# Kernel optimization log

Hardware: AMD Instinct MI355X
Metric: run time of the kernel (lower is better)

The kernel has to match this reference:

```python
import jax, jax.numpy as jnp
import numpy as np

B, L, D = 2, 1536, 1024
H, P = 16, 1024
HD = P // H  # 64
K_SIZE = 5
DIFF_STEPS = 3
ALPHA = 0.02
NEG = -1e9
EPS = 1e-9


def setup_inputs() -> dict:
    key = jax.random.key(0)
    ks = jax.random.split(key, 12)
    s = 0.02
    hidden_states = jax.random.normal(ks[0], (B, L, D), dtype=jnp.float32)
    attention_mask = jax.random.randint(ks[1], (B, L), 0, 2, dtype=jnp.int32)
    Wq = jax.random.normal(ks[2], (D, P), dtype=jnp.float32) * s
    bq = jax.random.normal(ks[3], (P,), dtype=jnp.float32) * s
    Wk = jax.random.normal(ks[4], (D, P), dtype=jnp.float32) * s
    bk = jax.random.normal(ks[5], (P,), dtype=jnp.float32) * s
    Wv = jax.random.normal(ks[6], (D, P), dtype=jnp.float32) * s
    bv = jax.random.normal(ks[7], (P,), dtype=jnp.float32) * s
    Wo = jax.random.normal(ks[8], (P, D), dtype=jnp.float32) * s
    bo = jax.random.normal(ks[9], (D,), dtype=jnp.float32) * s
    kernel_w = jax.random.normal(ks[10], (K_SIZE,), dtype=jnp.float32)
    return {"hidden_states": hidden_states, "attention_mask": attention_mask,
            "Wq": Wq, "bq": bq, "Wk": Wk, "bk": bk, "Wv": Wv, "bv": bv,
            "Wo": Wo, "bo": bo, "kernel_w": kernel_w}


def _causal_smooth(p, w):
    # p: (B,H,Lq,Lk); causal cross-correlation matching F.conv1d(pad=k-1)[:Lk]
    k = w.shape[0]
    Lk = p.shape[-1]
    pp = jnp.pad(p, ((0, 0), (0, 0), (0, 0), (k - 1, 0)))
    out = w[0] * pp[..., 0:Lk]
    for j in range(1, k):
        out = out + w[j] * pp[..., j:j + Lk]
    return out


def reference(hidden_states, attention_mask, Wq, bq, Wk, bk, Wv, bv, Wo, bo, kernel_w):
    mask_f = attention_mask.astype(hidden_states.dtype)  # (B,Lk), 1=keep
    additive = (1.0 - mask_f) * NEG                       # (B,Lk)
    key_valid = (attention_mask > 0).astype(hidden_states.dtype)

    Q = (hidden_states @ Wq + bq).reshape(B, L, H, HD)
    Kt = (hidden_states @ Wk + bk).reshape(B, L, H, HD)
    V = (hidden_states @ Wv + bv).reshape(B, L, H, HD)

    scores = jnp.einsum('bqhd,bkhd->bhqk', Q, Kt) / np.sqrt(HD).astype(np.float32)
    scores = scores + additive[:, None, None, :]
    p = jax.nn.softmax(scores, axis=-1)  # (B,H,Lq,Lk)

    w = jax.nn.softmax(kernel_w)  # (k,)
    kv4 = key_valid[:, None, None, :]
    for _ in range(DIFF_STEPS):
        ps = _causal_smooth(p, w)
        ps = ps * kv4
        ps = ps / (jnp.sum(ps, axis=-1, keepdims=True) + EPS)
        p = (1.0 - ALPHA) * p + ALPHA * ps

    attn = jnp.einsum('bhqk,bkhd->bqhd', p, V).reshape(B, L, P)
    return attn @ Wo + bo
```

## Files before the change

kernel.cpp:

```cpp
#include <hip/hip_runtime.h>

#define BB 2
#define LL 1536
#define DD 1024
#define HH 16
#define HDD 64
#define PP 1024

typedef __attribute__((ext_vector_type(8))) __bf16 bf16x8;
typedef __attribute__((ext_vector_type(4))) float f32x4;
typedef __attribute__((ext_vector_type(2))) float f32x2;
typedef _Float16 f16x2 __attribute__((ext_vector_type(2)));

__device__ __forceinline__ unsigned short f2b(float f) {
  unsigned int x = __builtin_bit_cast(unsigned int, f);
  unsigned int r = (x + 0x7FFFu + ((x >> 16) & 1u)) >> 16;
  return (unsigned short)r;
}
__device__ __forceinline__ bf16x8 ldb8(const unsigned short* p) {
  return __builtin_bit_cast(bf16x8, *(const uint4*)p);
}
__device__ __forceinline__ f32x2 mk2(float a, float b) {
  f32x2 r;
  r.x = a;
  r.y = b;
  return r;
}
__device__ __forceinline__ unsigned int cvtpk_bf16(float lo, float hi) {
  unsigned int r;
  asm("v_cvt_pk_bf16_f32 %0, %1, %2" : "=v"(r) : "v"(lo), "v"(hi));
  return r;
}
__device__ __forceinline__ float fdot2u(unsigned int a, unsigned int ones,
                                        float c) {
#if __has_builtin(__builtin_amdgcn_fdot2)
  return __builtin_amdgcn_fdot2(__builtin_bit_cast(f16x2, a),
                                __builtin_bit_cast(f16x2, ones), c, false);
#else
  f16x2 x = __builtin_bit_cast(f16x2, a);
  return c + (float)x.x + (float)x.y;
#endif
}
__device__ __forceinline__ void gl_lds16(const unsigned short* g,
                                         unsigned short* l) {
  __builtin_amdgcn_global_load_lds(
      (const __attribute__((address_space(1))) void*)g,
      (__attribute__((address_space(3))) void*)l, 16, 0, 0);
}

__global__ __launch_bounds__(256) void prep(
    const float* __restrict__ hs, unsigned short* __restrict__ hsb,
    const float* __restrict__ Wq, const float* __restrict__ Wk,
    const float* __restrict__ Wv, const float* __restrict__ Wo,
    unsigned short* __restrict__ WT) {
  const int bid = blockIdx.x;
  const int t = threadIdx.x;
  if (bid < 1536) {
    const int idx = bid * 2048 + t * 8;
    float4 a = *(const float4*)(hs + idx);
    float4 b = *(const float4*)(hs + idx + 4);
    uint4 u;
    u.x = (unsigned int)f2b(a.x) | ((unsigned int)f2b(a.y) << 16);
    u.y = (unsigned int)f2b(a.z) | ((unsigned int)f2b(a.w) << 16);
    u.z = (unsigned int)f2b(b.x) | ((unsigned int)f2b(b.y) << 16);
    u.w = (unsigned int)f2b(b.z) | ((unsigned int)f2b(b.w) << 16);
    *(uint4*)(hsb + idx) = u;
  } else {
    __shared__ float tile[64][68];
    const int t2 = bid - 1536;
    const int z = t2 >> 8;
    const int bx = t2 & 15, by = (t2 >> 4) & 15;
    const float* W = (z == 0) ? Wq : (z == 1) ? Wk : (z == 2) ? Wv : Wo;
    unsigned short* O = WT + (size_t)z * 1024 * 1024;
    const int r0 = by * 64;
    const int c0 = bx * 64;
#pragma unroll
    for (int i = 0; i < 4; ++i) {
      const int row = (t >> 4) + i * 16;
      const int col = (t & 15) * 4;
      *(float4*)&tile[row][col] =
          *(const float4*)&W[(size_t)(r0 + row) * 1024 + c0 + col];
    }
    __syncthreads();
#pragma unroll
    for (int i = 0; i < 4; ++i) {
      const int n = (t >> 4) + i * 16;
      const int k4 = (t & 15) * 4;
      uint2 u;
      u.x = (unsigned int)f2b(tile[k4 + 0][n]) |
            ((unsigned int)f2b(tile[k4 + 1][n]) << 16);
      u.y = (unsigned int)f2b(tile[k4 + 2][n]) |
            ((unsigned int)f2b(tile[k4 + 3][n]) << 16);
      *(uint2*)&O[(size_t)(c0 + n) * 1024 + r0 + k4] = u;
    }
  }
}

template <int MODE>
__device__ __forceinline__ void gemm_mfma_body(
    const unsigned short* __restrict__ A, const unsigned short* __restrict__ Bt,
    const float* __restrict__ bias, void* __restrict__ Cout) {
  __shared__ unsigned short As[128 * 32];
  __shared__ unsigned short Bs[128 * 32];
  const int t = threadIdx.x;
  const int lane = t & 63;
  const int w = t >> 6;
  const int quad = lane >> 4;
  const int lc = lane & 15;
  const int m0 = blockIdx.y * 128, n0 = blockIdx.x * 128;

  const int sr = lane >> 2;
  const int sk = (lane & 3) * 8;
  const unsigned short* ga0 = A + (size_t)(m0 + w * 32 + sr) * 1024 + sk;
  const unsigned short* ga1 = ga0 + 16 * 1024;
  const unsigned short* gb0 = Bt + (size_t)(n0 + w * 32 + sr) * 1024 + sk;
  const unsigned short* gb1 = gb0 + 16 * 1024;
  unsigned short* la0 = As + w * 1024;
  unsigned short* la1 = As + w * 1024 + 512;
  unsigned short* lb0 = Bs + w * 1024;
  unsigned short* lb1 = Bs + w * 1024 + 512;

  const int mrow0 = (w >> 1) * 64, ncol0 = (w & 1) * 64;

  f32x4 acc[4][4];
#pragma unroll
  for (int i = 0; i < 4; ++i)
#pragma unroll
    for (int j = 0; j < 4; ++j) acc[i][j] = (f32x4){0.f, 0.f, 0.f, 0.f};

  for (int k0 = 0; k0 < 1024; k0 += 32) {
    __syncthreads();
    gl_lds16(ga0 + k0, la0);
    gl_lds16(ga1 + k0, la1);
    gl_lds16(gb0 + k0, lb0);
    gl_lds16(gb1 + k0, lb1);
    __syncthreads();
    bf16x8 af[4], bfr[4];
#pragma unroll
    for (int i = 0; i < 4; ++i)
      af[i] = ldb8(&As[(mrow0 + i * 16 + lc) * 32 + quad * 8]);
#pragma unroll
    for (int j = 0; j < 4; ++j)
      bfr[j] = ldb8(&Bs[(ncol0 + j * 16 + lc) * 32 + quad * 8]);
#pragma unroll
    for (int i = 0; i < 4; ++i)
#pragma unroll
      for (int j = 0; j < 4; ++j)
        acc[i][j] = __builtin_amdgcn_mfma_f32_16x16x32_bf16(af[i], bfr[j],
                                                            acc[i][j], 0, 0, 0);
  }

#pragma unroll
  for (int i = 0; i < 4; ++i) {
    const int row0 = m0 + mrow0 + i * 16 + quad * 4;
#pragma unroll
    for (int jj = 0; jj < 4; ++jj) {
      const int col = n0 + ncol0 + jj * 16 + lc;
      const float bz = bias[col];
      float o[4];
#pragma unroll
      for (int r = 0; r < 4; ++r) o[r] = acc[i][jj][r] + bz;
      if constexpr (MODE == 0) {
        const int bb = row0 / LL;
        const int ql = row0 - bb * LL;
        const int qt = ql >> 4;
        const int m = ql & 15;
        const int hh = col >> 6;
        const int hd = col & 63;
        const int f = hd >> 5;
        const int qk = (hd >> 3) & 3;
        const int j = hd & 7;
        unsigned short* QF = (unsigned short*)Cout;
        const size_t base = (((size_t)(bb * HH + hh) * 96 + qt) * 2 + f) * 512 +
                            (qk * 16 + m) * 8 + j;
#pragma unroll
        for (int r = 0; r < 4; ++r) QF[base + r * 8] = f2b(o[r] * 0.125f);
      } else if constexpr (MODE == 1) {
        const int bb = row0 / LL;
        const int kl = row0 - bb * LL;
        const int ktl = kl >> 4;
        const int m = kl & 15;
        const int hh = col >> 6;
        const int hd = col & 63;
        const int f = hd >> 5;
        const int qk = (hd >> 3) & 3;
        const int j = hd & 7;
        unsigned short* KF = (unsigned short*)Cout;
        const size_t base =
            (((size_t)(bb * HH + hh) * 96 + ktl) * 2 + f) * 512 +
            (qk * 16 + m) * 8 + j;
#pragma unroll
        for (int r = 0; r < 4; ++r) KF[base + r * 8] = f2b(o[r]);
      } else if constexpr (MODE == 2) {
        const int bb = row0 / LL;
        const int kl = row0 - bb * LL;
        const int hh = col >> 6;
        const int hd = col & 63;
        const int hg = hd >> 4;
        const int lcv = hd & 15;
        const int tile = (kl >> 5);
        const int qv = (kl >> 3) & 3;
        const int j0 = kl & 7;
        unsigned short* VF = (unsigned short*)Cout;
        const size_t base = (((size_t)(bb * HH + hh) * 4 + hg) * 48 + tile) * 512 +
                            (qv * 16 + lcv) * 8 + j0;
        uint2 u;
        u.x = (unsigned int)f2b(o[0]) | ((unsigned int)f2b(o[1]) << 16);
        u.y = (unsigned int)f2b(o[2]) | ((unsigned int)f2b(o[3]) << 16);
        *(uint2*)&VF[base] = u;
      } else {
#pragma unroll
        for (int r = 0; r < 4; ++r)
          ((float*)Cout)[(size_t)(row0 + r) * 1024 + col] = o[r];
      }
    }
  }
}

__global__ __launch_bounds__(256) void qkv_gemm(
    const unsigned short* __restrict__ hsb,
    const unsigned short* __restrict__ WT, const float* __restrict__ bq,
    const float* __restrict__ bk, const float* __restrict__ bv,
    unsigned short* __restrict__ QF, unsigned short* __restrict__ KF,
    unsigned short* __restrict__ VF) {
  if (blockIdx.z == 0) {
    gemm_mfma_body<0>(hsb, WT, bq, QF);
  } else if (blockIdx.z == 1) {
    gemm_mfma_body<1>(hsb, WT + 1024 * 1024, bk, KF);
  } else {
    gemm_mfma_body<2>(hsb, WT + 2 * 1024 * 1024, bv, VF);
  }
}

__global__ __launch_bounds__(256) void out_gemm(
    const unsigned short* __restrict__ ctxb,
    const unsigned short* __restrict__ WoT, const float* __restrict__ bo,
    float* __restrict__ out) {
  gemm_mfma_body<3>(ctxb, WoT, bo, out);
}

__global__ __launch_bounds__(1024, 2) void attn_kernel(
    const unsigned short* __restrict__ QF,
    const unsigned short* __restrict__ KF,
    const unsigned short* __restrict__ VF, const int* __restrict__ mask,
    const float* __restrict__ kernel_w, unsigned short* __restrict__ ctxb) {
  __shared__ __align__(16) unsigned int P2u[97 * 128];
  __shared__ unsigned int kvb[48];
  __shared__ float red_s[16][16];
  __shared__ float wext[48];

  const int t = threadIdx.x;
  const int lane = t & 63;
  const int w = t >> 6;
  const int quad = lane >> 4;
  const int lc = lane & 15;
  const int b = blockIdx.z, h = blockIdx.y;
  const int q0 = blockIdx.x * 16;

  {
    unsigned long long bal = __ballot(mask[b * LL + t] > 0);
    if (lane == 0) {
      kvb[2 * w] = (unsigned int)bal;
      kvb[2 * w + 1] = (unsigned int)(bal >> 32);
    }
  }
  if (w < 8) {
    unsigned long long bal = __ballot(mask[b * LL + 1024 + t] > 0);
    if (lane == 0) {
      kvb[32 + 2 * w] = (unsigned int)bal;
      kvb[33 + 2 * w] = (unsigned int)(bal >> 32);
    }
  }
  if (t < 128) P2u[t] = 0;
  {
    float k0 = kernel_w[0], k1 = kernel_w[1], k2 = kernel_w[2],
          k3 = kernel_w[3], k4 = kernel_w[4];
    float km = fmaxf(fmaxf(fmaxf(k0, k1), fmaxf(k2, k3)), k4);
    float e0 = __expf(k0 - km), e1 = __expf(k1 - km), e2 = __expf(k2 - km),
          e3 = __expf(k3 - km), e4 = __expf(k4 - km);
    float es = e0 + e1 + e2 + e3 + e4;
    if (t < 48) {
      float v = 0.f;
      if (t == 16) v = e4 / es;
      if (t == 17) v = e3 / es;
      if (t == 18) v = e2 / es;
      if (t == 19) v = e1 / es;
      if (t == 20) v = e0 / es;
      wext[t] = v;
    }
  }
  __syncthreads();

  bf16x8 afb;
  {
    const int kb = lc + 32 - quad * 8;
    float bv[8];
#pragma unroll
    for (int jj = 0; jj < 8; ++jj) bv[jj] = wext[kb - jj];
    uint4 uu;
    uu.x = cvtpk_bf16(bv[0], bv[1]);
    uu.y = cvtpk_bf16(bv[2], bv[3]);
    uu.z = cvtpk_bf16(bv[4], bv[5]);
    uu.w = cvtpk_bf16(bv[6], bv[7]);
    afb = __builtin_bit_cast(bf16x8, uu);
  }

  const unsigned short* qfb =
      QF + (((size_t)(b * HH + h) * 96 + (q0 >> 4)) * 2) * 512 + lane * 8;
  const bf16x8 qb0 = ldb8(qfb);
  const bf16x8 qb1 = ldb8(qfb + 512);
  const unsigned short* kfb =
      KF + (((size_t)(b * HH + h) * 96 + 6 * w) * 2) * 512 + lane * 8;
  f32x2 pr[12];
#pragma unroll
  for (int j = 0; j < 6; ++j) {
    bf16x8 ka0 = ldb8(kfb + j * 1024);
    bf16x8 ka1 = ldb8(kfb + j * 1024 + 512);
    f32x4 acc = {0.f, 0.f, 0.f, 0.f};
    acc = __builtin_amdgcn_mfma_f32_16x16x32_bf16(ka0, qb0, acc, 0, 0, 0);
    acc = __builtin_amdgcn_mfma_f32_16x16x32_bf16(ka1, qb1, acc, 0, 0, 0);
    pr[2 * j] = mk2(acc[0], acc[1]);
    pr[2 * j + 1] = mk2(acc[2], acc[3]);
  }

  unsigned int mA = 0u;
  float s = 0.f;
#pragma unroll
  for (int j = 0; j < 6; ++j) {
    const int kb16 = 16 * j + 4 * quad;
    const unsigned int w4 = (kvb[3 * w + (kb16 >> 5)] >> (kb16 & 31)) & 0xFu;
    mA |= w4 << (4 * j);
    float e0 = (w4 & 1u) ? __expf(pr[2 * j].x) : 0.f;
    float e1 = (w4 & 2u) ? __expf(pr[2 * j].y) : 0.f;
    float e2 = (w4 & 4u) ? __expf(pr[2 * j + 1].x) : 0.f;
    float e3 = (w4 & 8u) ? __expf(pr[2 * j + 1].y) : 0.f;
    pr[2 * j] = mk2(e0, e1);
    pr[2 * j + 1] = mk2(e2, e3);
    s += (e0 + e1) + (e2 + e3);
  }
  s += __shfl_xor(s, 16, 64);
  s += __shfl_xor(s, 32, 64);
  if (lane < 16) red_s[w][lane] = s;
  __syncthreads();
  float tot0 = 0.f;
#pragma unroll
  for (int ww = 0; ww < 16; ++ww) tot0 += red_s[ww][lc];
  const float inv = 1.f / tot0;
#pragma unroll
  for (int i = 0; i < 12; ++i) pr[i] = pr[i] * inv;

  unsigned int* const pwb = &P2u[((6 * w + 1) * 16 + lc) * 8 + 2 * quad];
#pragma unroll
  for (int j = 0; j < 6; ++j) {
    uint2 u;
    u.x = cvtpk_bf16(pr[2 * j].x, pr[2 * j].y);
    u.y = cvtpk_bf16(pr[2 * j + 1].x, pr[2 * j + 1].y);
    *(uint2*)(pwb + j * 128) = u;
  }
  __syncthreads();

  const unsigned int ones2 = 0x3C003C00u;
  const unsigned int* const prb =
      &P2u[((6 * w + (quad >> 1)) * 16 + lc) * 8 + (quad & 1) * 4];
#pragma unroll
  for (int step = 0; step < 3; ++step) {
    unsigned int s_pk[12];
    float sum = 0.f;
#pragma unroll
    for (int j = 0; j < 6; ++j) {
      bf16x8 bfr = ldb8((const unsigned short*)(prb + j * 128));
      f32x4 z = {0.f, 0.f, 0.f, 0.f};
      f32x4 ps = __builtin_amdgcn_mfma_f32_16x16x32_bf16(afb, bfr, z, 0, 0, 0);
      const unsigned int w4 = (mA >> (4 * j)) & 0xFu;
      float p0 = (w4 & 1u) ? ps[0] : 0.f;
      float p1 = (w4 & 2u) ? ps[1] : 0.f;
      float p2 = (w4 & 4u) ? ps[2] : 0.f;
      float p3 = (w4 & 8u) ? ps[3] : 0.f;
      s_pk[2 * j] =
          __builtin_bit_cast(unsigned int, __builtin_amdgcn_cvt_pkrtz(p0, p1));
      s_pk[2 * j + 1] =
          __builtin_bit_cast(unsigned int, __builtin_amdgcn_cvt_pkrtz(p2, p3));
      sum = fdot2u(s_pk[2 * j], ones2, sum);
      sum = fdot2u(s_pk[2 * j + 1], ones2, sum);
    }
    sum += __shfl_xor(sum, 16, 64);
    sum += __shfl_xor(sum, 32, 64);
    if (lane < 16) red_s[w][lane] = sum;
    __syncthreads();
    float tot = 0.f;
#pragma unroll
    for (int ww = 0; ww < 16; ++ww) tot += red_s[ww][lc];
    const float pinv = 0.02f / (tot + 1e-9f);
#pragma unroll
    for (int i = 0; i < 12; ++i) {
      f16x2 hp = __builtin_bit_cast(f16x2, s_pk[i]);
      pr[i] = pr[i] * 0.98f + mk2((float)hp.x, (float)hp.y) * pinv;
    }
#pragma unroll
    for (int j = 0; j < 6; ++j) {
      uint2 u;
      u.x = cvtpk_bf16(pr[2 * j].x, pr[2 * j].y);
      u.y = cvtpk_bf16(pr[2 * j + 1].x, pr[2 * j + 1].y);
      *(uint2*)(pwb + j * 128) = u;
    }
    __syncthreads();
  }

  const int cg = w & 3;
  const int kt = w >> 2;
  const int cidx = cg * 16 + lc;
  const unsigned short* vfb =
      VF + ((((size_t)(b * HH + h) * 4 + cg) * 48 + 12 * kt) * 512) + lane * 8;
  const unsigned int* const pvb =
      &P2u[((24 * kt + 1 + (quad >> 1)) * 16 + lc) * 8 + (quad & 1) * 4];
  f32x4 oacc = {0.f, 0.f, 0.f, 0.f};
#pragma unroll
  for (int g = 0; g < 6; ++g) {
#pragma unroll
    for (int c = 0; c < 2; ++c) {
      bf16x8 pa = ldb8((const unsigned short*)(pvb + (4 * g + 2 * c) * 128));
      bf16x8 vf = ldb8(vfb + (2 * g + c) * 512);
      oacc = __builtin_amdgcn_mfma_f32_16x16x32_bf16(pa, vf, oacc, 0, 0, 0);
    }
  }
  __syncthreads();
  float* pscr = (float*)&P2u[0];
  if (kt > 0) {
    const int idx = (kt - 1) * 4096 + ((cg * 4 + quad) * 16 + lc) * 4;
    *(float4*)(pscr + idx) = make_float4(oacc[0], oacc[1], oacc[2], oacc[3]);
  }
  __syncthreads();
  if (kt == 0) {
    float o[4] = {oacc[0], oacc[1], oacc[2], oacc[3]};
#pragma unroll
    for (int p = 0; p < 3; ++p) {
      const int idx = p * 4096 + ((cg * 4 + quad) * 16 + lc) * 4;
      float4 prr = *(const float4*)(pscr + idx);
      o[0] += prr.x;
      o[1] += prr.y;
      o[2] += prr.z;
      o[3] += prr.w;
    }
#pragma unroll
    for (int r = 0; r < 4; ++r)
      ctxb[((size_t)(b * LL + q0 + quad * 4 + r)) * PP + h * HDD + cidx] =
          f2b(o[r]);
  }
}

extern "C" void kernel_launch(void* const* d_in, const int* in_sizes, int n_in,
                              void* d_out, int out_size, void* d_ws,
                              size_t ws_size, hipStream_t stream) {
  const float* hs = (const float*)d_in[0];
  const int* mask = (const int*)d_in[1];
  const float* Wq = (const float*)d_in[2];
  const float* bq = (const float*)d_in[3];
  const float* Wk = (const float*)d_in[4];
  const float* bk = (const float*)d_in[5];
  const float* Wv = (const float*)d_in[6];
  const float* bv = (const float*)d_in[7];
  const float* Wo = (const float*)d_in[8];
  const float* bo = (const float*)d_in[9];
  const float* kw = (const float*)d_in[10];

  const size_t NBLP = (size_t)BB * LL * PP;
  unsigned short* QF = (unsigned short*)d_ws;
  unsigned short* KF = QF + NBLP;
  unsigned short* VF = KF + NBLP;
  unsigned short* ctxb = VF + NBLP;
  unsigned short* hsb = ctxb + NBLP;
  unsigned short* WT = hsb + NBLP;

  dim3 blk(256);
  prep<<<dim3(2560), blk, 0, stream>>>(hs, hsb, Wq, Wk, Wv, Wo, WT);
  qkv_gemm<<<dim3(8, 24, 3), blk, 0, stream>>>(hsb, WT, bq, bk, bv, QF, KF, VF);
  attn_kernel<<<dim3(96, 16, 2), dim3(1024), 0, stream>>>(QF, KF, VF, mask, kw,
                                                          ctxb);
  out_gemm<<<dim3(8, 24, 1), blk, 0, stream>>>(ctxb, WT + 3 * 1024 * 1024, bo,
                                               (float*)d_out);
}
```

Before: 280.2 us.

## Switch attention diffusion to fp16 packed math and defer softmax normalization

Attention probabilities are now kept as packed fp16 in registers, and the diffusion update uses packed f16x2 arithmetic instead of fp32 with bf16 repacking. The smoothing and PV matmuls move from bf16 MFMA to f16 MFMA, and V is stored as fp16. The softmax normalization no longer has its own barrier: the unnormalized exponentials are written first and scaled inside the first diffusion step, using double-buffered reduction arrays. This removes one barrier and many conversion instructions, at the cost of fp16 range and precision risks, since unnormalized exps can overflow fp16.

After: 276.3 us. No clear change (-1.4%).

```diff
diff --git a/kernel.cpp b/kernel.cpp
--- a/kernel.cpp
+++ b/kernel.cpp
@@ -11,6 +11,7 @@
 typedef __attribute__((ext_vector_type(4))) float f32x4;
 typedef __attribute__((ext_vector_type(2))) float f32x2;
 typedef _Float16 f16x2 __attribute__((ext_vector_type(2)));
+typedef _Float16 f16x8 __attribute__((ext_vector_type(8)));
 
 __device__ __forceinline__ unsigned short f2b(float f) {
   unsigned int x = __builtin_bit_cast(unsigned int, f);
@@ -19,6 +20,9 @@
 }
 __device__ __forceinline__ bf16x8 ldb8(const unsigned short* p) {
   return __builtin_bit_cast(bf16x8, *(const uint4*)p);
+}
+__device__ __forceinline__ f16x8 ldh8u(const unsigned int* p) {
+  return __builtin_bit_cast(f16x8, *(const uint4*)p);
 }
 __device__ __forceinline__ f32x2 mk2(float a, float b) {
   f32x2 r;
@@ -26,10 +30,8 @@
   r.y = b;
   return r;
 }
-__device__ __forceinline__ unsigned int cvtpk_bf16(float lo, float hi) {
-  unsigned int r;
-  asm("v_cvt_pk_bf16_f32 %0, %1, %2" : "=v"(r) : "v"(lo), "v"(hi));
-  return r;
+__device__ __forceinline__ unsigned int pkrtz(float lo, float hi) {
+  return __builtin_bit_cast(unsigned int, __builtin_amdgcn_cvt_pkrtz(lo, hi));
 }
 __device__ __forceinline__ float fdot2u(unsigned int a, unsigned int ones,
                                         float c) {
@@ -205,8 +207,8 @@
         const size_t base = (((size_t)(bb * HH + hh) * 4 + hg) * 48 + tile) * 512 +
                             (qv * 16 + lcv) * 8 + j0;
         uint2 u;
-        u.x = (unsigned int)f2b(o[0]) | ((unsigned int)f2b(o[1]) << 16);
-        u.y = (unsigned int)f2b(o[2]) | ((unsigned int)f2b(o[3]) << 16);
+        u.x = pkrtz(o[0], o[1]);
+        u.y = pkrtz(o[2], o[3]);
         *(uint2*)&VF[base] = u;
       } else {
 #pragma unroll
@@ -246,7 +248,8 @@
     const float* __restrict__ kernel_w, unsigned short* __restrict__ ctxb) {
   __shared__ __align__(16) unsigned int P2u[97 * 128];
   __shared__ unsigned int kvb[48];
-  __shared__ float red_s[16][16];
+  __shared__ float red_a[16][16];
+  __shared__ float red_b[16][16];
   __shared__ float wext[48];
 
   const int t = threadIdx.x;
@@ -291,18 +294,15 @@
   }
   __syncthreads();
 
-  bf16x8 afb;
+  f16x8 afb;
   {
     const int kb = lc + 32 - quad * 8;
-    float bv[8];
-#pragma unroll
-    for (int jj = 0; jj < 8; ++jj) bv[jj] = wext[kb - jj];
     uint4 uu;
-    uu.x = cvtpk_bf16(bv[0], bv[1]);
-    uu.y = cvtpk_bf16(bv[2], bv[3]);
-    uu.z = cvtpk_bf16(bv[4], bv[5]);
-    uu.w = cvtpk_bf16(bv[6], bv[7]);
-    afb = __builtin_bit_cast(bf16x8, uu);
+    uu.x = pkrtz(wext[kb], wext[kb - 1]);
+    uu.y = pkrtz(wext[kb - 2], wext[kb - 3]);
+    uu.z = pkrtz(wext[kb - 4], wext[kb - 5]);
+    uu.w = pkrtz(wext[kb - 6], wext[kb - 7]);
+    afb = __builtin_bit_cast(f16x8, uu);
   }
 
   const unsigned short* qfb =
@@ -311,7 +311,8 @@
   const bf16x8 qb1 = ldb8(qfb + 512);
   const unsigned short* kfb =
       KF + (((size_t)(b * HH + h) * 96 + 6 * w) * 2) * 512 + lane * 8;
-  f32x2 pr[12];
+  f32x2 sc[6];
+  f32x2 sc2[6];
 #pragma unroll
   for (int j = 0; j < 6; ++j) {
     bf16x8 ka0 = ldb8(kfb + j * 1024);
@@ -319,10 +320,11 @@
     f32x4 acc = {0.f, 0.f, 0.f, 0.f};
     acc = __builtin_amdgcn_mfma_f32_16x16x32_bf16(ka0, qb0, acc, 0, 0, 0);
     acc = __builtin_amdgcn_mfma_f32_16x16x32_bf16(ka1, qb1, acc, 0, 0, 0);
-    pr[2 * j] = mk2(acc[0], acc[1]);
-    pr[2 * j + 1] = mk2(acc[2], acc[3]);
-  }
-
+    sc[j] = mk2(acc[0], acc[1]);
+    sc2[j] = mk2(acc[2], acc[3]);
+  }
+
+  unsigned int prq[12];
   unsigned int mA = 0u;
   float s = 0.f;
 #pragma unroll
@@ -330,77 +332,104 @@
     const int kb16 = 16 * j + 4 * quad;
     const unsigned int w4 = (kvb[3 * w + (kb16 >> 5)] >> (kb16 & 31)) & 0xFu;
     mA |= w4 << (4 * j);
-    float e0 = (w4 & 1u) ? __expf(pr[2 * j].x) : 0.f;
-    float e1 = (w4 & 2u) ? __expf(pr[2 * j].y) : 0.f;
-    float e2 = (w4 & 4u) ? __expf(pr[2 * j + 1].x) : 0.f;
-    float e3 = (w4 & 8u) ? __expf(pr[2 * j + 1].y) : 0.f;
-    pr[2 * j] = mk2(e0, e1);
-    pr[2 * j + 1] = mk2(e2, e3);
+    float e0 = (w4 & 1u) ? __expf(sc[j].x) : 0.f;
+    float e1 = (w4 & 2u) ? __expf(sc[j].y) : 0.f;
+    float e2 = (w4 & 4u) ? __expf(sc2[j].x) : 0.f;
+    float e3 = (w4 & 8u) ? __expf(sc2[j].y) : 0.f;
+    prq[2 * j] = pkrtz(e0, e1);
+    prq[2 * j + 1] = pkrtz(e2, e3);
     s += (e0 + e1) + (e2 + e3);
   }
   s += __shfl_xor(s, 16, 64);
   s += __shfl_xor(s, 32, 64);
-  if (lane < 16) red_s[w][lane] = s;
-  __syncthreads();
-  float tot0 = 0.f;
-#pragma unroll
-  for (int ww = 0; ww < 16; ++ww) tot0 += red_s[ww][lc];
-  const float inv = 1.f / tot0;
-#pragma unroll
-  for (int i = 0; i < 12; ++i) pr[i] = pr[i] * inv;
+  if (lane < 16) red_a[w][lane] = s;
 
   unsigned int* const pwb = &P2u[((6 * w + 1) * 16 + lc) * 8 + 2 * quad];
 #pragma unroll
   for (int j = 0; j < 6; ++j) {
     uint2 u;
-    u.x = cvtpk_bf16(pr[2 * j].x, pr[2 * j].y);
-    u.y = cvtpk_bf16(pr[2 * j + 1].x, pr[2 * j + 1].y);
+    u.x = prq[2 * j];
+    u.y = prq[2 * j + 1];
     *(uint2*)(pwb + j * 128) = u;
   }
   __syncthreads();
 
   const unsigned int ones2 = 0x3C003C00u;
+  const f16x2 c98 = {(_Float16)0.98f, (_Float16)0.98f};
   const unsigned int* const prb =
       &P2u[((6 * w + (quad >> 1)) * 16 + lc) * 8 + (quad & 1) * 4];
+  float inv = 0.f;
 #pragma unroll
   for (int step = 0; step < 3; ++step) {
     unsigned int s_pk[12];
     float sum = 0.f;
 #pragma unroll
     for (int j = 0; j < 6; ++j) {
-      bf16x8 bfr = ldb8((const unsigned short*)(prb + j * 128));
+      f16x8 bfr = ldh8u(prb + j * 128);
       f32x4 z = {0.f, 0.f, 0.f, 0.f};
-      f32x4 ps = __builtin_amdgcn_mfma_f32_16x16x32_bf16(afb, bfr, z, 0, 0, 0);
+      f32x4 ps = __builtin_amdgcn_mfma_f32_16x16x32_f16(afb, bfr, z, 0, 0, 0);
       const unsigned int w4 = (mA >> (4 * j)) & 0xFu;
       float p0 = (w4 & 1u) ? ps[0] : 0.f;
       float p1 = (w4 & 2u) ? ps[1] : 0.f;
       float p2 = (w4 & 4u) ? ps[2] : 0.f;
       float p3 = (w4 & 8u) ? ps[3] : 0.f;
-      s_pk[2 * j] =
-          __builtin_bit_cast(unsigned int, __builtin_amdgcn_cvt_pkrtz(p0, p1));
-      s_pk[2 * j + 1] =
-          __builtin_bit_cast(unsigned int, __builtin_amdgcn_cvt_pkrtz(p2, p3));
+      s_pk[2 * j] = pkrtz(p0, p1);
+      s_pk[2 * j + 1] = pkrtz(p2, p3);
       sum = fdot2u(s_pk[2 * j], ones2, sum);
       sum = fdot2u(s_pk[2 * j + 1], ones2, sum);
     }
     sum += __shfl_xor(sum, 16, 64);
     sum += __shfl_xor(sum, 32, 64);
-    if (lane < 16) red_s[w][lane] = sum;
+    if (step == 0) {
+      float tot0 = 0.f;
+#pragma unroll
+      for (int ww = 0; ww < 16; ++ww) tot0 += red_a[ww][lc];
+      inv = 1.f / tot0;
+    }
+    if (lane < 16) {
+      if (step & 1)
+        red_a[w][lane] = sum;
+      else
+        red_b[w][lane] = sum;
+    }
     __syncthreads();
     float tot = 0.f;
 #pragma unroll
-    for (int ww = 0; ww < 16; ++ww) tot += red_s[ww][lc];
-    const float pinv = 0.02f / (tot + 1e-9f);
-#pragma unroll
-    for (int i = 0; i < 12; ++i) {
-      f16x2 hp = __builtin_bit_cast(f16x2, s_pk[i]);
-      pr[i] = pr[i] * 0.98f + mk2((float)hp.x, (float)hp.y) * pinv;
+    for (int ww = 0; ww < 16; ++ww)
+      tot += (step & 1) ? red_a[ww][lc] : red_b[ww][lc];
+    if (step == 0) {
+      const float sps = tot * inv;
+      const float pinv = 0.02f / (sps + 1e-9f);
+      const _Float16 hi = (_Float16)inv;
+      const _Float16 hc = (_Float16)(0.98f * inv);
+      const _Float16 hp = (_Float16)pinv;
+      const f16x2 inv2 = {hi, hi};
+      const f16x2 c1 = {hc, hc};
+      const f16x2 pv2 = {hp, hp};
+#pragma unroll
+      for (int i = 0; i < 12; ++i) {
+        f16x2 ph = __builtin_bit_cast(f16x2, prq[i]);
+        f16x2 sh = __builtin_bit_cast(f16x2, s_pk[i]);
+        ph = ph * c1 + (sh * inv2) * pv2;
+        prq[i] = __builtin_bit_cast(unsigned int, ph);
+      }
+    } else {
+      const float pinv = 0.02f / (tot + 1e-9f);
+      const _Float16 hp = (_Float16)pinv;
+      const f16x2 pv2 = {hp, hp};
+#pragma unroll
+      for (int i = 0; i < 12; ++i) {
+        f16x2 ph = __builtin_bit_cast(f16x2, prq[i]);
+        f16x2 sh = __builtin_bit_cast(f16x2, s_pk[i]);
+        ph = ph * c98 + sh * pv2;
+        prq[i] = __builtin_bit_cast(unsigned int, ph);
+      }
     }
 #pragma unroll
     for (int j = 0; j < 6; ++j) {
       uint2 u;
-      u.x = cvtpk_bf16(pr[2 * j].x, pr[2 * j].y);
-      u.y = cvtpk_bf16(pr[2 * j + 1].x, pr[2 * j + 1].y);
+      u.x = prq[2 * j];
+      u.y = prq[2 * j + 1];
       *(uint2*)(pwb + j * 128) = u;
     }
     __syncthreads();
@@ -418,9 +447,9 @@
   for (int g = 0; g < 6; ++g) {
 #pragma unroll
     for (int c = 0; c < 2; ++c) {
-      bf16x8 pa = ldb8((const unsigned short*)(pvb + (4 * g + 2 * c) * 128));
-      bf16x8 vf = ldb8(vfb + (2 * g + c) * 512);
-      oacc = __builtin_amdgcn_mfma_f32_16x16x32_bf16(pa, vf, oacc, 0, 0, 0);
+      f16x8 pa = ldh8u(pvb + (4 * g + 2 * c) * 128);
+      f16x8 vf = __builtin_bit_cast(f16x8, *(const uint4*)(vfb + (2 * g + c) * 512));
+      oacc = __builtin_amdgcn_mfma_f32_16x16x32_f16(pa, vf, oacc, 0, 0, 0);
     }
   }
   __syncthreads();
```
